# Optimization experiments

Measured on AMD Instinct MI355X. Metric: run time of the kernel, lower is better.

The kernel has to match this reference:

```python
import math
import jax, jax.numpy as jnp
import numpy as np

B, C, H, W = 16, 128, 128, 128  # width == dim required by nn.LayerNorm(dim) on (b,c,h,w)
HEADS, DIM_HEAD = 8, 32
INNER = HEADS * DIM_HEAD


def _ln_last(x, g, b, eps=1e-5):
    # torch nn.LayerNorm over the LAST axis (here: width), biased variance
    mu = x.mean(-1, keepdims=True)
    var = x.var(-1, keepdims=True)
    return (x - mu) * jax.lax.rsqrt(var + eps) * g + b


def setup_inputs() -> dict:
    key = jax.random.key(0)
    k0, k1, k2 = jax.random.split(key, 3)
    return {
        "fmap": jax.random.normal(k0, (B, C, H, W), jnp.float32),
        "ln0_g": jnp.ones((C,), jnp.float32),
        "ln0_b": jnp.zeros((C,), jnp.float32),
        "w_qkv": jax.random.normal(k1, (3 * INNER, C), jnp.float32) * 0.05,
        "w_out": jax.random.normal(k2, (C, INNER), jnp.float32) * 0.05,
        "ln1_g": jnp.ones((C,), jnp.float32),
        "ln1_b": jnp.zeros((C,), jnp.float32),
    }


def reference(fmap, ln0_g, ln0_b, w_qkv, w_out, ln1_g, ln1_b):
    b, c, x, y = fmap.shape
    n = x * y
    scale = DIM_HEAD ** -0.5

    fm = _ln_last(fmap, ln0_g, ln0_b)
    # 1x1 conv (no bias) == channel matmul
    qkv = jnp.einsum('bcxy,oc->boxy', fm, w_qkv)  # (b, 3*inner, x, y)
    q, k, v = jnp.split(qkv, 3, axis=1)

    def to_heads(t):
        # b (h c) x y -> (b h) (x y) c
        return t.reshape(b, HEADS, DIM_HEAD, n).transpose(0, 1, 3, 2).reshape(b * HEADS, n, DIM_HEAD)

    q, k, v = map(to_heads, (q, k, v))

    q = jax.nn.softmax(q, axis=-1) * scale
    k = jax.nn.softmax(k, axis=-2)
    # l2norm(v) along feature dim (F.normalize, eps=1e-12)
    v = v / jnp.clip(jnp.linalg.norm(v, axis=-1, keepdims=True), 1e-12)
    inv = 1.0 / math.sqrt(n)
    k = k * inv
    v = v * inv

    context = jnp.einsum('bnd,bne->bde', k, v)   # small (d=32, e=32) context
    out = jnp.einsum('bnd,bde->bne', q, context)

    # (b h) (x y) d -> b (h d) x y
    out = out.reshape(b, HEADS, n, DIM_HEAD).transpose(0, 1, 3, 2).reshape(b, INNER, x, y)
    out = jax.nn.gelu(out, approximate=False)  # torch nn.GELU default (erf)
    out = jnp.einsum('bcxy,oc->boxy', out, w_out)  # 1x1 conv, no bias
    return _ln_last(out, ln1_g, ln1_b)
```

## Files before the change

kernel.cpp:

```cpp
#include <hip/hip_runtime.h>
#include <math.h>

#define OFF_MU    0u
#define OFF_RSTD  262144u
#define OFF_CTXA  524288u
#define OFF_CTXP  2686976u
#define OFF_WSPL  2883584u
#define OFF_WQSPL 2981888u
#define OFF_WOSPL 3031040u

typedef __attribute__((ext_vector_type(8))) short bf16x8;
typedef __attribute__((ext_vector_type(4))) float f32x4;

__device__ __forceinline__ void split3(float v, unsigned& h, unsigned& m, unsigned& l) {
  unsigned u = __float_as_uint(v);
  float r1 = v - __uint_as_float(u & 0xffff0000u);
  unsigned u1 = __float_as_uint(r1);
  float r2 = r1 - __uint_as_float(u1 & 0xffff0000u);
  h = u >> 16; m = u1 >> 16; l = __float_as_uint(r2) >> 16;
}

__device__ __forceinline__ f32x4 mfma6(const bf16x8& A0, const bf16x8& A1, const bf16x8& A2,
                                       const bf16x8& B0, const bf16x8& B1, const bf16x8& B2,
                                       f32x4 c) {
  c = __builtin_amdgcn_mfma_f32_16x16x32_bf16(A0, B0, c, 0, 0, 0);
  c = __builtin_amdgcn_mfma_f32_16x16x32_bf16(A0, B1, c, 0, 0, 0);
  c = __builtin_amdgcn_mfma_f32_16x16x32_bf16(A1, B0, c, 0, 0, 0);
  c = __builtin_amdgcn_mfma_f32_16x16x32_bf16(A0, B2, c, 0, 0, 0);
  c = __builtin_amdgcn_mfma_f32_16x16x32_bf16(A1, B1, c, 0, 0, 0);
  c = __builtin_amdgcn_mfma_f32_16x16x32_bf16(A2, B0, c, 0, 0, 0);
  return c;
}

__global__ void prep_kernel(const float* __restrict__ wqkv,
                            const float* __restrict__ wout,
                            float* __restrict__ ws) {
  int idx = blockIdx.x * 256 + threadIdx.x;
  float v;
  unsigned short* wp;
  unsigned plane, slot;
  if (idx < 65536) {
    int row = idx >> 7, c = idx & 127;
    int blk = row >> 7, ol = row & 127;
    int hh = (ol >> 5) & 1;
    int src = ((ol & 64) ? 512 : 256) + (2 * blk + hh) * 32 + (ol & 31);
    v = wqkv[src * 128 + c];
    wp = (unsigned short*)(ws + OFF_WSPL);
    plane = 65536; slot = (unsigned)idx;
  } else if (idx < 98304) {
    int j = idx - 65536;
    v = wqkv[j];
    wp = (unsigned short*)(ws + OFF_WQSPL);
    plane = 32768; slot = (unsigned)j;
  } else {
    int j = idx - 98304;
    int o = j >> 8, k = j & 255;
    int cp = (k & 0xE0) | (((k >> 2) & 1) << 4) | (((k >> 3) & 3) << 2) | (k & 3);
    v = wout[o * 256 + cp];
    wp = (unsigned short*)(ws + OFF_WOSPL);
    plane = 32768; slot = (unsigned)j;
  }
  unsigned h, m, l;
  split3(v, h, m, l);
  wp[slot]             = (unsigned short)h;
  wp[plane + slot]     = (unsigned short)m;
  wp[2 * plane + slot] = (unsigned short)l;
}

__launch_bounds__(512, 4)
__global__ void kv_ctx_kernel(const float* __restrict__ fmap,
                              const float* __restrict__ g0,
                              const float* __restrict__ b0,
                              float* __restrict__ ws) {
  __shared__ float sm[13888];
  const int x = blockIdx.x, b = blockIdx.y, t = threadIdx.x;
  const int wave = t >> 6, lane = t & 63;
  const int ln = lane & 15, kb = lane >> 4;
  const int or2 = wave >> 1, yc = wave & 1;
  const int dt = lane >> 3, et = lane & 7;
  const int xg = x >> 3;

  float* pb  = sm;
  float* vb  = sm + 2304;
  float* vss = sm + 4608;
  float* ser = sm + 4864;
  float* rnS = sm + 5120;
  float* red = sm + 5184;
  float* pls = sm + 5184;
  float* muS = sm + 13376;
  float* rsS = sm + 13504;
  float* g0S = sm + 13632;
  float* b0S = sm + 13760;
  float* fmS = sm;

  {
    const int r = t >> 2, q = t & 3;
    const float* p = fmap + (((size_t)(b * 128 + r)) * 128 + x) * 128 + q * 32;
    double s = 0.0, qq = 0.0;
    #pragma unroll
    for (int i = 0; i < 8; ++i) {
      float4 v4 = *(const float4*)(p + i * 4);
      s  += (double)v4.x + (double)v4.y + (double)v4.z + (double)v4.w;
      qq += (double)v4.x * v4.x + (double)v4.y * v4.y
          + (double)v4.z * v4.z + (double)v4.w * v4.w;
    }
    s += __shfl_xor(s, 1); qq += __shfl_xor(qq, 1);
    s += __shfl_xor(s, 2); qq += __shfl_xor(qq, 2);
    if (q == 0) {
      double mu = s * (1.0 / 128.0);
      double var = qq * (1.0 / 128.0) - mu * mu;
      float muf = (float)mu, rsf = (float)(1.0 / sqrt(var + 1e-5));
      muS[r] = muf; rsS[r] = rsf;
      ws[OFF_MU + (unsigned)((b * 128 + r) * 128 + x)] = muf;
      ws[OFF_RSTD + (unsigned)((b * 128 + r) * 128 + x)] = rsf;
    }
  }
  if (t < 128) { g0S[t] = g0[t]; b0S[t] = b0[t]; }

  const unsigned short* wspl = (const unsigned short*)(ws + OFF_WSPL);

  for (int blk = 0; blk < 4; ++blk) {
    f32x4 acc[2][4];
    #pragma unroll
    for (int i = 0; i < 2; ++i)
      #pragma unroll
      for (int j = 0; j < 4; ++j) acc[i][j] = (f32x4){0.f, 0.f, 0.f, 0.f};

    for (int cc = 0; cc < 4; ++cc) {
      bf16x8 af[2][3];
      #pragma unroll
      for (int ot = 0; ot < 2; ++ot)
        #pragma unroll
        for (int p = 0; p < 3; ++p)
          af[ot][p] = *(const bf16x8*)(wspl + p * 65536 +
              ((blk * 128 + or2 * 32 + ot * 16 + ln) * 128 + cc * 32 + kb * 8));

      __syncthreads();
      #pragma unroll
      for (int it = 0; it < 2; ++it) {
        int idx4 = it * 512 + t;
        int c = idx4 >> 5, y4 = (idx4 & 31) * 4;
        int cg = cc * 32 + c;
        const float4 r = *(const float4*)(fmap + (((size_t)(b * 128 + cg)) * 128 + x) * 128 + y4);
        float mu = muS[cg], rs = rsS[cg];
        float4 g = *(const float4*)(g0S + y4);
        float4 be = *(const float4*)(b0S + y4);
        float4 o;
        o.x = (r.x - mu) * rs * g.x + be.x;
        o.y = (r.y - mu) * rs * g.y + be.y;
        o.z = (r.z - mu) * rs * g.z + be.z;
        o.w = (r.w - mu) * rs * g.w + be.w;
        *(float4*)(fmS + c * 128 + y4) = o;
      }
      __syncthreads();
      {
        const int ty = t & 127, cg = t >> 7;
        unsigned int d0[4], d1[4], d2[4];
        #pragma unroll
        for (int jj = 0; jj < 4; ++jj) {
          unsigned int h[2], m[2], l[2];
          #pragma unroll
          for (int e = 0; e < 2; ++e) {
            float v = fmS[(cg * 8 + jj * 2 + e) * 128 + ty];
            split3(v, h[e], m[e], l[e]);
          }
          d0[jj] = h[0] | (h[1] << 16);
          d1[jj] = m[0] | (m[1] << 16);
          d2[jj] = l[0] | (l[1] << 16);
        }
        float* pp = pls + ty * 20 + cg * 4;
        *reinterpret_cast<uint4*>(pp)        = make_uint4(d0[0], d0[1], d0[2], d0[3]);
        *reinterpret_cast<uint4*>(pp + 2560) = make_uint4(d1[0], d1[1], d1[2], d1[3]);
        *reinterpret_cast<uint4*>(pp + 5120) = make_uint4(d2[0], d2[1], d2[2], d2[3]);
      }
      __syncthreads();
      #pragma unroll
      for (int yt = 0; yt < 4; ++yt) {
        const float* bp = pls + ((yc * 4 + yt) * 16 + ln) * 20 + kb * 4;
        bf16x8 B0 = *(const bf16x8*)(bp);
        bf16x8 B1 = *(const bf16x8*)(bp + 2560);
        bf16x8 B2 = *(const bf16x8*)(bp + 5120);
        #pragma unroll
        for (int ot = 0; ot < 2; ++ot)
          acc[ot][yt] = mfma6(af[ot][0], af[ot][1], af[ot][2], B0, B1, B2, acc[ot][yt]);
      }
    }

    for (int hh = 0; hh < 2; ++hh) {
      float u[16], se[4];
      #pragma unroll
      for (int i = 0; i < 16; ++i) u[i] = 0.0f;
      se[0] = se[1] = se[2] = se[3] = 0.0f;

      for (int hf = 0; hf < 2; ++hf) {
        if (wave == hh * 2 + hf) {
          #pragma unroll
          for (int ot = 0; ot < 2; ++ot)
            #pragma unroll
            for (int yt = 0; yt < 4; ++yt) {
              f32x4 a = acc[ot][yt];
              float4 p;
              p.x = __expf(a[0]); p.y = __expf(a[1]);
              p.z = __expf(a[2]); p.w = __expf(a[3]);
              *(float4*)(pb + (yt * 16 + ln) * 36 + ot * 16 + kb * 4) = p;
            }
        }
        if (wave == 4 + hh * 2 + hf) {
          #pragma unroll
          for (int yt = 0; yt < 4; ++yt) {
            f32x4 a0 = acc[0][yt], a1 = acc[1][yt];
            int yl = yt * 16 + ln;
            *(float4*)(vb + yl * 36 + kb * 4)      = make_float4(a0[0], a0[1], a0[2], a0[3]);
            *(float4*)(vb + yl * 36 + 16 + kb * 4) = make_float4(a1[0], a1[1], a1[2], a1[3]);
            float s = a0[0] * a0[0] + a0[1] * a0[1] + a0[2] * a0[2] + a0[3] * a0[3]
                    + a1[0] * a1[0] + a1[1] * a1[1] + a1[2] * a1[2] + a1[3] * a1[3];
            vss[kb * 64 + yl] = s;
          }
        }
        __syncthreads();
        if (t < 64) {
          float s2 = vss[t] + vss[64 + t] + vss[128 + t] + vss[192 + t];
          rnS[t] = 1.0f / fmaxf(sqrtf(s2), 1e-12f);
        }
        __syncthreads();
        #pragma unroll 2
        for (int yy = 0; yy < 8; ++yy) {
          int y = wave * 8 + yy;
          const float4 p = *(const float4*)(pb + y * 36 + dt * 4);
          float4 v = *(const float4*)(vb + y * 36 + et * 4);
          float rn = rnS[y];
          v.x *= rn; v.y *= rn; v.z *= rn; v.w *= rn;
          se[0] += p.x; se[1] += p.y; se[2] += p.z; se[3] += p.w;
          u[0]  = fmaf(p.x, v.x, u[0]);  u[1]  = fmaf(p.x, v.y, u[1]);
          u[2]  = fmaf(p.x, v.z, u[2]);  u[3]  = fmaf(p.x, v.w, u[3]);
          u[4]  = fmaf(p.y, v.x, u[4]);  u[5]  = fmaf(p.y, v.y, u[5]);
          u[6]  = fmaf(p.y, v.z, u[6]);  u[7]  = fmaf(p.y, v.w, u[7]);
          u[8]  = fmaf(p.z, v.x, u[8]);  u[9]  = fmaf(p.z, v.y, u[9]);
          u[10] = fmaf(p.z, v.z, u[10]); u[11] = fmaf(p.z, v.w, u[11]);
          u[12] = fmaf(p.w, v.x, u[12]); u[13] = fmaf(p.w, v.y, u[13]);
          u[14] = fmaf(p.w, v.z, u[14]); u[15] = fmaf(p.w, v.w, u[15]);
        }
        __syncthreads();
      }
      *(float4*)(red + t * 16 + 0)  = make_float4(u[0], u[1], u[2], u[3]);
      *(float4*)(red + t * 16 + 4)  = make_float4(u[4], u[5], u[6], u[7]);
      *(float4*)(red + t * 16 + 8)  = make_float4(u[8], u[9], u[10], u[11]);
      *(float4*)(red + t * 16 + 12) = make_float4(u[12], u[13], u[14], u[15]);
      if (et == 0)
        *(float4*)(ser + (wave * 8 + dt) * 4) = make_float4(se[0], se[1], se[2], se[3]);
      __syncthreads();
      {
        const int tile = t >> 3;
        const int i0 = (t & 7) * 2;
        float s0 = 0.0f, s1 = 0.0f;
        #pragma unroll
        for (int w = 0; w < 8; ++w) {
          s0 += red[(w * 64 + tile) * 16 + i0];
          s1 += red[(w * 64 + tile) * 16 + i0 + 1];
        }
        const int d = (tile >> 3) * 4 + (i0 >> 2);
        const int e = (tile & 7) * 4 + (i0 & 3);
        float* ca = ws + OFF_CTXA + ((size_t)(b * 8 + blk * 2 + hh) * 16 + xg) * 1056;
        atomicAdd(ca + d * 32 + e, s0);
        atomicAdd(ca + d * 32 + e + 1, s1);
        if (t < 32) {
          float ss = 0.0f;
          #pragma unroll
          for (int w = 0; w < 8; ++w) ss += ser[(w * 8 + (t >> 2)) * 4 + (t & 3)];
          atomicAdd(ca + 1024 + t, ss);
        }
      }
    }
  }
}

__global__ void ctx_reduce_kernel(float* __restrict__ ws) {
  __shared__ float sume[32];
  const int bh = blockIdx.x, t = threadIdx.x;
  const float* ca = ws + OFF_CTXA + (size_t)bh * 16 * 1056;
  if (t < 32) {
    double a = 0.0;
    #pragma unroll
    for (int xg = 0; xg < 16; ++xg) a += ca[xg * 1056 + 1024 + t];
    sume[t] = (float)a;
  }
  __syncthreads();
  const double sb = (1.0 / 16384.0) * 0.17677669529663688;
  unsigned short* cp = (unsigned short*)(ws + OFF_CTXP) + (size_t)bh * 3072;
  #pragma unroll
  for (int i = 0; i < 4; ++i) {
    int de = t + 256 * i;
    int d = de >> 5, e = de & 31;
    double a = 0.0;
    #pragma unroll
    for (int xg = 0; xg < 16; ++xg) a += ca[xg * 1056 + de];
    float v = (float)(a * sb / (double)sume[d]);
    int k = ((d >> 2) & 3) * 8 + ((d >> 4) & 1) * 4 + (d & 3);
    unsigned h, m, l;
    split3(v, h, m, l);
    cp[e * 32 + k]        = (unsigned short)h;
    cp[1024 + e * 32 + k] = (unsigned short)m;
    cp[2048 + e * 32 + k] = (unsigned short)l;
  }
}

__launch_bounds__(512, 2)
__global__ void final_kernel(const float* __restrict__ fmap,
                             const float* __restrict__ g0,
                             const float* __restrict__ b0,
                             const float* __restrict__ g1,
                             const float* __restrict__ b1,
                             const float* __restrict__ ws,
                             float* __restrict__ out) {
  __shared__ float sm[14592];
  const int x = blockIdx.x, b = blockIdx.y, t = threadIdx.x;
  const int wave = t >> 6, lane = t & 63;
  const int ln = lane & 15, kb = lane >> 4;
  const int or2 = wave >> 1, yc = wave & 1;

  float* fmS = sm;
  float* pls = sm + 4096;
  float* gel = sm;
  float* muS = sm + 13824;
  float* rsS = sm + 13952;
  float* g0S = sm + 14080;
  float* b0S = sm + 14208;
  float* lnm = sm + 14336;
  float* lnr = sm + 14464;

  if (t < 128) {
    muS[t] = ws[OFF_MU + (unsigned)((b * 128 + t) * 128 + x)];
    rsS[t] = ws[OFF_RSTD + (unsigned)((b * 128 + t) * 128 + x)];
  } else if (t < 256) g0S[t - 128] = g0[t - 128];
  else if (t < 384) b0S[t - 256] = b0[t - 256];

  const unsigned short* wqspl = (const unsigned short*)(ws + OFF_WQSPL);
  const unsigned short* wospl = (const unsigned short*)(ws + OFF_WOSPL);
  const unsigned short* ctxp  = (const unsigned short*)(ws + OFF_CTXP);

  f32x4 oacc[2][4];
  #pragma unroll
  for (int i = 0; i < 2; ++i)
    #pragma unroll
    for (int j = 0; j < 4; ++j) oacc[i][j] = (f32x4){0.f, 0.f, 0.f, 0.f};

  for (int qblk = 0; qblk < 2; ++qblk) {
    f32x4 qacc[2][4];
    #pragma unroll
    for (int i = 0; i < 2; ++i)
      #pragma unroll
      for (int j = 0; j < 4; ++j) qacc[i][j] = (f32x4){0.f, 0.f, 0.f, 0.f};

    for (int cc = 0; cc < 4; ++cc) {
      bf16x8 af[2][3];
      #pragma unroll
      for (int ot = 0; ot < 2; ++ot)
        #pragma unroll
        for (int p = 0; p < 3; ++p)
          af[ot][p] = *(const bf16x8*)(wqspl + p * 32768 +
              ((qblk * 128 + or2 * 32 + ot * 16 + ln) * 128 + cc * 32 + kb * 8));

      __syncthreads();
      #pragma unroll
      for (int it = 0; it < 2; ++it) {
        int idx4 = it * 512 + t;
        int c = idx4 >> 5, y4 = (idx4 & 31) * 4;
        int cg = cc * 32 + c;
        const float4 r = *(const float4*)(fmap + (((size_t)(b * 128 + cg)) * 128 + x) * 128 + y4);
        float mu = muS[cg], rs = rsS[cg];
        float4 g = *(const float4*)(g0S + y4);
        float4 be = *(const float4*)(b0S + y4);
        float4 o;
        o.x = (r.x - mu) * rs * g.x + be.x;
        o.y = (r.y - mu) * rs * g.y + be.y;
        o.z = (r.z - mu) * rs * g.z + be.z;
        o.w = (r.w - mu) * rs * g.w + be.w;
        *(float4*)(fmS + c * 128 + y4) = o;
      }
      __syncthreads();
      {
        const int ty = t & 127, cg = t >> 7;
        unsigned int d0[4], d1[4], d2[4];
        #pragma unroll
        for (int jj = 0; jj < 4; ++jj) {
          unsigned int h[2], m[2], l[2];
          #pragma unroll
          for (int e = 0; e < 2; ++e) {
            float v = fmS[(cg * 8 + jj * 2 + e) * 128 + ty];
            split3(v, h[e], m[e], l[e]);
          }
          d0[jj] = h[0] | (h[1] << 16);
          d1[jj] = m[0] | (m[1] << 16);
          d2[jj] = l[0] | (l[1] << 16);
        }
        float* pp = pls + ty * 20 + cg * 4;
        *reinterpret_cast<uint4*>(pp)        = make_uint4(d0[0], d0[1], d0[2], d0[3]);
        *reinterpret_cast<uint4*>(pp + 2560) = make_uint4(d1[0], d1[1], d1[2], d1[3]);
        *reinterpret_cast<uint4*>(pp + 5120) = make_uint4(d2[0], d2[1], d2[2], d2[3]);
      }
      __syncthreads();
      #pragma unroll
      for (int yt = 0; yt < 4; ++yt) {
        const float* bp = pls + ((yc * 4 + yt) * 16 + ln) * 20 + kb * 4;
        bf16x8 B0 = *(const bf16x8*)(bp);
        bf16x8 B1 = *(const bf16x8*)(bp + 2560);
        bf16x8 B2 = *(const bf16x8*)(bp + 5120);
        #pragma unroll
        for (int ot = 0; ot < 2; ++ot)
          qacc[ot][yt] = mfma6(af[ot][0], af[ot][1], af[ot][2], B0, B1, B2, qacc[ot][yt]);
      }
    }

    float rssum[4];
    bf16x8 pf0[4], pf1[4], pf2[4];
    #pragma unroll
    for (int yt = 0; yt < 4; ++yt) {
      float pv[8];
      #pragma unroll
      for (int ot = 0; ot < 2; ++ot)
        #pragma unroll
        for (int r = 0; r < 4; ++r)
          pv[ot * 4 + r] = __expf(qacc[ot][yt][r]);
      float ps = ((pv[0] + pv[1]) + (pv[2] + pv[3])) + ((pv[4] + pv[5]) + (pv[6] + pv[7]));
      ps += __shfl_xor(ps, 16);
      ps += __shfl_xor(ps, 32);
      rssum[yt] = 1.0f / ps;
      unsigned wh[4], wm[4], wl[4];
      #pragma unroll
      for (int j = 0; j < 4; ++j) {
        unsigned h0, m0, l0, h1, m1, l1;
        split3(pv[2 * j], h0, m0, l0);
        split3(pv[2 * j + 1], h1, m1, l1);
        wh[j] = h0 | (h1 << 16);
        wm[j] = m0 | (m1 << 16);
        wl[j] = l0 | (l1 << 16);
      }
      uint4 uh = make_uint4(wh[0], wh[1], wh[2], wh[3]);
      uint4 um = make_uint4(wm[0], wm[1], wm[2], wm[3]);
      uint4 ul = make_uint4(wl[0], wl[1], wl[2], wl[3]);
      pf0[yt] = *(const bf16x8*)&uh;
      pf1[yt] = *(const bf16x8*)&um;
      pf2[yt] = *(const bf16x8*)&ul;
    }

    f32x4 ge[2][4];
    const unsigned short* chp = ctxp + (size_t)(b * 8 + qblk * 4 + or2) * 3072;
    #pragma unroll
    for (int ot = 0; ot < 2; ++ot) {
      bf16x8 aq0 = *(const bf16x8*)(chp +        (ot * 16 + ln) * 32 + kb * 8);
      bf16x8 aq1 = *(const bf16x8*)(chp + 1024 + (ot * 16 + ln) * 32 + kb * 8);
      bf16x8 aq2 = *(const bf16x8*)(chp + 2048 + (ot * 16 + ln) * 32 + kb * 8);
      #pragma unroll
      for (int yt = 0; yt < 4; ++yt) {
        f32x4 c = (f32x4){0.f, 0.f, 0.f, 0.f};
        ge[ot][yt] = mfma6(aq0, aq1, aq2, pf0[yt], pf1[yt], pf2[yt], c);
      }
    }

    #pragma unroll
    for (int ot = 0; ot < 2; ++ot)
      #pragma unroll
      for (int yt = 0; yt < 4; ++yt)
        #pragma unroll
        for (int r = 0; r < 4; ++r) {
          float v = ge[ot][yt][r] * rssum[yt];
          ge[ot][yt][r] = 0.5f * v * (1.0f + erff(v * 0.70710678118654752f));
        }

    for (int ph = 0; ph < 2; ++ph) {
      __syncthreads();
      if ((or2 >> 1) == ph) {
        const int c16 = (or2 & 1) * 16;
        #pragma unroll
        for (int yt = 0; yt < 4; ++yt) {
          float* grow = gel + ((yc * 4 + yt) * 16 + ln) * 36 + c16 + kb * 4;
          #pragma unroll
          for (int ot = 0; ot < 2; ++ot) {
            unsigned h0, m0, l0, h1, m1, l1, h2, m2, l2, h3, m3, l3;
            split3(ge[ot][yt][0], h0, m0, l0);
            split3(ge[ot][yt][1], h1, m1, l1);
            split3(ge[ot][yt][2], h2, m2, l2);
            split3(ge[ot][yt][3], h3, m3, l3);
            *(uint2*)(grow + ot * 2)        = make_uint2(h0 | (h1 << 16), h2 | (h3 << 16));
            *(uint2*)(grow + 4608 + ot * 2) = make_uint2(m0 | (m1 << 16), m2 | (m3 << 16));
            *(uint2*)(grow + 9216 + ot * 2) = make_uint2(l0 | (l1 << 16), l2 | (l3 << 16));
          }
        }
      }
      __syncthreads();
      #pragma unroll
      for (int kc = 0; kc < 2; ++kc) {
        bf16x8 ao[2][3];
        #pragma unroll
        for (int ot = 0; ot < 2; ++ot)
          #pragma unroll
          for (int p = 0; p < 3; ++p)
            ao[ot][p] = *(const bf16x8*)(wospl + p * 32768 +
                ((or2 * 32 + ot * 16 + ln) * 256 + qblk * 128 + ph * 64 + kc * 32 + kb * 8));
        #pragma unroll
        for (int yt = 0; yt < 4; ++yt) {
          const float* bp = gel + ((yc * 4 + yt) * 16 + ln) * 36 + kc * 16 + kb * 4;
          bf16x8 B0 = *(const bf16x8*)(bp);
          bf16x8 B1 = *(const bf16x8*)(bp + 4608);
          bf16x8 B2 = *(const bf16x8*)(bp + 9216);
          #pragma unroll
          for (int ot = 0; ot < 2; ++ot)
            oacc[ot][yt] = mfma6(ao[ot][0], ao[ot][1], ao[ot][2], B0, B1, B2, oacc[ot][yt]);
        }
      }
    }
  }

  __syncthreads();
  float* red_s = sm;
  float* red_q = sm + 4096;
  #pragma unroll
  for (int ot = 0; ot < 2; ++ot)
    #pragma unroll
    for (int r = 0; r < 4; ++r) {
      int o = or2 * 32 + ot * 16 + kb * 4 + r;
      float s = 0.0f, q = 0.0f;
      #pragma unroll
      for (int yt = 0; yt < 4; ++yt) { float v = oacc[ot][yt][r]; s += v; q = fmaf(v, v, q); }
      red_s[o * 32 + yc * 16 + ln] = s;
      red_q[o * 32 + yc * 16 + ln] = q;
    }
  __syncthreads();
  if (t < 128) {
    double s = 0.0, q = 0.0;
    #pragma unroll
    for (int i = 0; i < 32; ++i) { s += red_s[t * 32 + i]; q += red_q[t * 32 + i]; }
    double mu = s * (1.0 / 128.0);
    double var = q * (1.0 / 128.0) - mu * mu;
    lnm[t] = (float)mu;
    lnr[t] = (float)(1.0 / sqrt(var + 1e-5));
  }
  __syncthreads();
  float g1v[4], b1v[4];
  #pragma unroll
  for (int yt = 0; yt < 4; ++yt) {
    int y = (yc * 4 + yt) * 16 + ln;
    g1v[yt] = g1[y]; b1v[yt] = b1[y];
  }
  #pragma unroll
  for (int ot = 0; ot < 2; ++ot)
    #pragma unroll
    for (int r = 0; r < 4; ++r) {
      int o = or2 * 32 + ot * 16 + kb * 4 + r;
      float mu = lnm[o], rs = lnr[o];
      #pragma unroll
      for (int yt = 0; yt < 4; ++yt) {
        int y = (yc * 4 + yt) * 16 + ln;
        out[(((size_t)(b * 128 + o)) * 128 + x) * 128 + y] =
            (oacc[ot][yt][r] - mu) * rs * g1v[yt] + b1v[yt];
      }
    }
}

extern "C" void kernel_launch(void* const* d_in, const int* in_sizes, int n_in,
                              void* d_out, int out_size, void* d_ws, size_t ws_size,
                              hipStream_t stream) {
  const float* fmap = (const float*)d_in[0];
  const float* g0   = (const float*)d_in[1];
  const float* b0   = (const float*)d_in[2];
  const float* wqkv = (const float*)d_in[3];
  const float* wout = (const float*)d_in[4];
  const float* g1   = (const float*)d_in[5];
  const float* b1   = (const float*)d_in[6];
  float* ws  = (float*)d_ws;
  float* out = (float*)d_out;

  hipMemsetAsync((char*)d_ws + (size_t)OFF_CTXA * 4, 0, (size_t)2162688 * 4, stream);
  prep_kernel<<<512, 256, 0, stream>>>(wqkv, wout, ws);
  kv_ctx_kernel<<<dim3(128, 16), 512, 0, stream>>>(fmap, g0, b0, ws);
  ctx_reduce_kernel<<<128, 256, 0, stream>>>(ws);
  final_kernel<<<dim3(128, 16), 512, 0, stream>>>(fmap, g0, b0, g1, b1, ws, out);
}
```

Measured before the change: 883.9 us.

## Compute all KV blocks in one pass over fmap and process two heads per step

The kv_ctx kernel now keeps accumulators for all four k/v output blocks in registers, so each fmap chunk is loaded, layer-normalised and split into bf16 planes once instead of four times. The softmax/context stage then handles two heads at once, using all 8 waves over 32 rows each, which halves the number of barrier-separated phases. To fit this, launch bounds drop to 2 blocks per SM and shared memory grows to about 80KB. The cost is higher register pressure (32 accumulator vectors) and lower occupancy.

Measured after the change: 872.3 us. About the same (-1.3%).

```diff
diff --git a/kernel.cpp b/kernel.cpp
--- a/kernel.cpp
+++ b/kernel.cpp
@@ -67,12 +67,12 @@
   wp[2 * plane + slot] = (unsigned short)l;
 }
 
-__launch_bounds__(512, 4)
+__launch_bounds__(512, 2)
 __global__ void kv_ctx_kernel(const float* __restrict__ fmap,
                               const float* __restrict__ g0,
                               const float* __restrict__ b0,
                               float* __restrict__ ws) {
-  __shared__ float sm[13888];
+  __shared__ float sm[19968];
   const int x = blockIdx.x, b = blockIdx.y, t = threadIdx.x;
   const int wave = t >> 6, lane = t & 63;
   const int ln = lane & 15, kb = lane >> 4;
@@ -80,18 +80,18 @@
   const int dt = lane >> 3, et = lane & 7;
   const int xg = x >> 3;
 
+  float* fmS = sm;
+  float* pls = sm + 4096;
+  float* muS = sm + 11776;
+  float* rsS = sm + 11904;
+  float* g0S = sm + 12032;
+  float* b0S = sm + 12160;
   float* pb  = sm;
-  float* vb  = sm + 2304;
-  float* vss = sm + 4608;
-  float* ser = sm + 4864;
-  float* rnS = sm + 5120;
-  float* red = sm + 5184;
-  float* pls = sm + 5184;
-  float* muS = sm + 13376;
-  float* rsS = sm + 13504;
-  float* g0S = sm + 13632;
-  float* b0S = sm + 13760;
-  float* fmS = sm;
+  float* vb  = sm + 9216;
+  float* vss = sm + 18432;
+  float* rnS = sm + 19456;
+  float* ser = sm + 19712;
+  float* red = sm;
 
   {
     const int r = t >> 2, q = t & 3;
@@ -119,12 +119,263 @@
 
   const unsigned short* wspl = (const unsigned short*)(ws + OFF_WSPL);
 
+  f32x4 acc[4][2][4];
+  #pragma unroll
+  for (int k = 0; k < 4; ++k)
+    #pragma unroll
+    for (int i = 0; i < 2; ++i)
+      #pragma unroll
+      for (int j = 0; j < 4; ++j) acc[k][i][j] = (f32x4){0.f, 0.f, 0.f, 0.f};
+
+  for (int cc = 0; cc < 4; ++cc) {
+    __syncthreads();
+    #pragma unroll
+    for (int it = 0; it < 2; ++it) {
+      int idx4 = it * 512 + t;
+      int c = idx4 >> 5, y4 = (idx4 & 31) * 4;
+      int cg = cc * 32 + c;
+      const float4 r = *(const float4*)(fmap + (((size_t)(b * 128 + cg)) * 128 + x) * 128 + y4);
+      float mu = muS[cg], rs = rsS[cg];
+      float4 g = *(const float4*)(g0S + y4);
+      float4 be = *(const float4*)(b0S + y4);
+      float4 o;
+      o.x = (r.x - mu) * rs * g.x + be.x;
+      o.y = (r.y - mu) * rs * g.y + be.y;
+      o.z = (r.z - mu) * rs * g.z + be.z;
+      o.w = (r.w - mu) * rs * g.w + be.w;
+      *(float4*)(fmS + c * 128 + y4) = o;
+    }
+    __syncthreads();
+    {
+      const int ty = t & 127, cg = t >> 7;
+      unsigned int d0[4], d1[4], d2[4];
+      #pragma unroll
+      for (int jj = 0; jj < 4; ++jj) {
+        unsigned int h[2], m[2], l[2];
+        #pragma unroll
+        for (int e = 0; e < 2; ++e) {
+          float v = fmS[(cg * 8 + jj * 2 + e) * 128 + ty];
+          split3(v, h[e], m[e], l[e]);
+        }
+        d0[jj] = h[0] | (h[1] << 16);
+        d1[jj] = m[0] | (m[1] << 16);
+        d2[jj] = l[0] | (l[1] << 16);
+      }
+      float* pp = pls + ty * 20 + cg * 4;
+      *reinterpret_cast<uint4*>(pp)        = make_uint4(d0[0], d0[1], d0[2], d0[3]);
+      *reinterpret_cast<uint4*>(pp + 2560) = make_uint4(d1[0], d1[1], d1[2], d1[3]);
+      *reinterpret_cast<uint4*>(pp + 5120) = make_uint4(d2[0], d2[1], d2[2], d2[3]);
+    }
+    __syncthreads();
+    #pragma unroll
+    for (int pg = 0; pg < 2; ++pg) {
+      bf16x8 af[2][2][3];
+      #pragma unroll
+      for (int bb = 0; bb < 2; ++bb)
+        #pragma unroll
+        for (int ot = 0; ot < 2; ++ot)
+          #pragma unroll
+          for (int p = 0; p < 3; ++p)
+            af[bb][ot][p] = *(const bf16x8*)(wspl + p * 65536 +
+                (((pg * 2 + bb) * 128 + or2 * 32 + ot * 16 + ln) * 128 + cc * 32 + kb * 8));
+      #pragma unroll
+      for (int yt = 0; yt < 4; ++yt) {
+        const float* bp = pls + ((yc * 4 + yt) * 16 + ln) * 20 + kb * 4;
+        bf16x8 B0 = *(const bf16x8*)(bp);
+        bf16x8 B1 = *(const bf16x8*)(bp + 2560);
+        bf16x8 B2 = *(const bf16x8*)(bp + 5120);
+        #pragma unroll
+        for (int bb = 0; bb < 2; ++bb)
+          #pragma unroll
+          for (int ot = 0; ot < 2; ++ot)
+            acc[pg * 2 + bb][ot][yt] =
+                mfma6(af[bb][ot][0], af[bb][ot][1], af[bb][ot][2], B0, B1, B2,
+                      acc[pg * 2 + bb][ot][yt]);
+      }
+    }
+  }
+
+  #pragma unroll
   for (int blk = 0; blk < 4; ++blk) {
-    f32x4 acc[2][4];
+    __syncthreads();
+    if (or2 < 2) {
+      const int h = or2;
+      #pragma unroll
+      for (int ot = 0; ot < 2; ++ot)
+        #pragma unroll
+        for (int yt = 0; yt < 4; ++yt) {
+          f32x4 a = acc[blk][ot][yt];
+          float4 p;
+          p.x = __expf(a[0]); p.y = __expf(a[1]);
+          p.z = __expf(a[2]); p.w = __expf(a[3]);
+          *(float4*)(pb + h * 4608 + ((yc * 4 + yt) * 16 + ln) * 36 + ot * 16 + kb * 4) = p;
+        }
+    } else {
+      const int h = or2 - 2;
+      #pragma unroll
+      for (int yt = 0; yt < 4; ++yt) {
+        f32x4 a0 = acc[blk][0][yt], a1 = acc[blk][1][yt];
+        int y = (yc * 4 + yt) * 16 + ln;
+        *(float4*)(vb + h * 4608 + y * 36 + kb * 4)      = make_float4(a0[0], a0[1], a0[2], a0[3]);
+        *(float4*)(vb + h * 4608 + y * 36 + 16 + kb * 4) = make_float4(a1[0], a1[1], a1[2], a1[3]);
+        float s = a0[0] * a0[0] + a0[1] * a0[1] + a0[2] * a0[2] + a0[3] * a0[3]
+                + a1[0] * a1[0] + a1[1] * a1[1] + a1[2] * a1[2] + a1[3] * a1[3];
+        vss[h * 512 + kb * 128 + y] = s;
+      }
+    }
+    __syncthreads();
+    if (t < 256) {
+      int h = t >> 7, y = t & 127;
+      const float* vh = vss + h * 512;
+      float s2 = vh[y] + vh[128 + y] + vh[256 + y] + vh[384 + y];
+      rnS[h * 128 + y] = 1.0f / fmaxf(sqrtf(s2), 1e-12f);
+    }
+    __syncthreads();
+    float u[16], se[4];
+    #pragma unroll
+    for (int i = 0; i < 16; ++i) u[i] = 0.0f;
+    se[0] = se[1] = se[2] = se[3] = 0.0f;
+    {
+      const int h = wave >> 2, yb = (wave & 3) * 32;
+      const float* pbh = pb + h * 4608;
+      const float* vbh = vb + h * 4608;
+      const float* rnh = rnS + h * 128;
+      #pragma unroll 4
+      for (int yy = 0; yy < 32; ++yy) {
+        int y = yb + yy;
+        const float4 p = *(const float4*)(pbh + y * 36 + dt * 4);
+        float4 v = *(const float4*)(vbh + y * 36 + et * 4);
+        float rn = rnh[y];
+        v.x *= rn; v.y *= rn; v.z *= rn; v.w *= rn;
+        se[0] += p.x; se[1] += p.y; se[2] += p.z; se[3] += p.w;
+        u[0]  = fmaf(p.x, v.x, u[0]);  u[1]  = fmaf(p.x, v.y, u[1]);
+        u[2]  = fmaf(p.x, v.z, u[2]);  u[3]  = fmaf(p.x, v.w, u[3]);
+        u[4]  = fmaf(p.y, v.x, u[4]);  u[5]  = fmaf(p.y, v.y, u[5]);
+        u[6]  = fmaf(p.y, v.z, u[6]);  u[7]  = fmaf(p.y, v.w, u[7]);
+        u[8]  = fmaf(p.z, v.x, u[8]);  u[9]  = fmaf(p.z, v.y, u[9]);
+        u[10] = fmaf(p.z, v.z, u[10]); u[11] = fmaf(p.z, v.w, u[11]);
+        u[12] = fmaf(p.w, v.x, u[12]); u[13] = fmaf(p.w, v.y, u[13]);
+        u[14] = fmaf(p.w, v.z, u[14]); u[15] = fmaf(p.w, v.w, u[15]);
+      }
+    }
+    __syncthreads();
+    {
+      const int h = wave >> 2;
+      float* rp = red + h * 4096 + ((wave & 3) * 64 + lane) * 16;
+      *(float4*)(rp + 0)  = make_float4(u[0], u[1], u[2], u[3]);
+      *(float4*)(rp + 4)  = make_float4(u[4], u[5], u[6], u[7]);
+      *(float4*)(rp + 8)  = make_float4(u[8], u[9], u[10], u[11]);
+      *(float4*)(rp + 12) = make_float4(u[12], u[13], u[14], u[15]);
+      if (et == 0)
+        *(float4*)(ser + h * 128 + ((wave & 3) * 8 + dt) * 4) = make_float4(se[0], se[1], se[2], se[3]);
+    }
+    __syncthreads();
+    {
+      const int tile = t >> 3, i0 = (t & 7) * 2;
+      const int d = (tile >> 3) * 4 + (i0 >> 2);
+      const int e = (tile & 7) * 4 + (i0 & 3);
+      #pragma unroll
+      for (int h = 0; h < 2; ++h) {
+        const float* rh = red + h * 4096;
+        float s0 = 0.0f, s1 = 0.0f;
+        #pragma unroll
+        for (int w4 = 0; w4 < 4; ++w4) {
+          s0 += rh[(w4 * 64 + tile) * 16 + i0];
+          s1 += rh[(w4 * 64 + tile) * 16 + i0 + 1];
+        }
+        float* ca = ws + OFF_CTXA + ((size_t)(b * 8 + blk * 2 + h) * 16 + xg) * 1056;
+        atomicAdd(ca + d * 32 + e, s0);
+        atomicAdd(ca + d * 32 + e + 1, s1);
+      }
+      if (t < 64) {
+        int h = t >> 5, tq = t & 31;
+        float ss = 0.0f;
+        #pragma unroll
+        for (int w4 = 0; w4 < 4; ++w4)
+          ss += ser[h * 128 + (w4 * 8 + (tq >> 2)) * 4 + (tq & 3)];
+        float* ca = ws + OFF_CTXA + ((size_t)(b * 8 + blk * 2 + h) * 16 + xg) * 1056;
+        atomicAdd(ca + 1024 + tq, ss);
+      }
+    }
+  }
+}
+
+__global__ void ctx_reduce_kernel(float* __restrict__ ws) {
+  __shared__ float sume[32];
+  const int bh = blockIdx.x, t = threadIdx.x;
+  const float* ca = ws + OFF_CTXA + (size_t)bh * 16 * 1056;
+  if (t < 32) {
+    double a = 0.0;
+    #pragma unroll
+    for (int xg = 0; xg < 16; ++xg) a += ca[xg * 1056 + 1024 + t];
+    sume[t] = (float)a;
+  }
+  __syncthreads();
+  const double sb = (1.0 / 16384.0) * 0.17677669529663688;
+  unsigned short* cp = (unsigned short*)(ws + OFF_CTXP) + (size_t)bh * 3072;
+  #pragma unroll
+  for (int i = 0; i < 4; ++i) {
+    int de = t + 256 * i;
+    int d = de >> 5, e = de & 31;
+    double a = 0.0;
+    #pragma unroll
+    for (int xg = 0; xg < 16; ++xg) a += ca[xg * 1056 + de];
+    float v = (float)(a * sb / (double)sume[d]);
+    int k = ((d >> 2) & 3) * 8 + ((d >> 4) & 1) * 4 + (d & 3);
+    unsigned h, m, l;
+    split3(v, h, m, l);
+    cp[e * 32 + k]        = (unsigned short)h;
+    cp[1024 + e * 32 + k] = (unsigned short)m;
+    cp[2048 + e * 32 + k] = (unsigned short)l;
+  }
+}
+
+__launch_bounds__(512, 2)
+__global__ void final_kernel(const float* __restrict__ fmap,
+                             const float* __restrict__ g0,
+                             const float* __restrict__ b0,
+                             const float* __restrict__ g1,
+                             const float* __restrict__ b1,
+                             const float* __restrict__ ws,
+                             float* __restrict__ out) {
+  __shared__ float sm[14592];
+  const int x = blockIdx.x, b = blockIdx.y, t = threadIdx.x;
+  const int wave = t >> 6, lane = t & 63;
+  const int ln = lane & 15, kb = lane >> 4;
+  const int or2 = wave >> 1, yc = wave & 1;
+
+  float* fmS = sm;
+  float* pls = sm + 4096;
+  float* gel = sm;
+  float* muS = sm + 13824;
+  float* rsS = sm + 13952;
+  float* g0S = sm + 14080;
+  float* b0S = sm + 14208;
+  float* lnm = sm + 14336;
+  float* lnr = sm + 14464;
+
+  if (t < 128) {
+    muS[t] = ws[OFF_MU + (unsigned)((b * 128 + t) * 128 + x)];
+    rsS[t] = ws[OFF_RSTD + (unsigned)((b * 128 + t) * 128 + x)];
+  } else if (t < 256) g0S[t - 128] = g0[t - 128];
+  else if (t < 384) b0S[t - 256] = b0[t - 256];
+
+  const unsigned short* wqspl = (const unsigned short*)(ws + OFF_WQSPL);
+  const unsigned short* wospl = (const unsigned short*)(ws + OFF_WOSPL);
+  const unsigned short* ctxp  = (const unsigned short*)(ws + OFF_CTXP);
+
+  f32x4 oacc[2][4];
+  #pragma unroll
+  for (int i = 0; i < 2; ++i)
+    #pragma unroll
+    for (int j = 0; j < 4; ++j) oacc[i][j] = (f32x4){0.f, 0.f, 0.f, 0.f};
+
+  for (int qblk = 0; qblk < 2; ++qblk) {
+    f32x4 qacc[2][4];
     #pragma unroll
     for (int i = 0; i < 2; ++i)
       #pragma unroll
-      for (int j = 0; j < 4; ++j) acc[i][j] = (f32x4){0.f, 0.f, 0.f, 0.f};
+      for (int j = 0; j < 4; ++j) qacc[i][j] = (f32x4){0.f, 0.f, 0.f, 0.f};
 
     for (int cc = 0; cc < 4; ++cc) {
       bf16x8 af[2][3];
@@ -132,8 +383,8 @@
       for (int ot = 0; ot < 2; ++ot)
         #pragma unroll
         for (int p = 0; p < 3; ++p)
-          af[ot][p] = *(const bf16x8*)(wspl + p * 65536 +
-              ((blk * 128 + or2 * 32 + ot * 16 + ln) * 128 + cc * 32 + kb * 8));
+          af[ot][p] = *(const bf16x8*)(wqspl + p * 32768 +
+              ((qblk * 128 + or2 * 32 + ot * 16 + ln) * 128 + cc * 32 + kb * 8));
 
       __syncthreads();
       #pragma unroll
@@ -182,231 +433,6 @@
         bf16x8 B2 = *(const bf16x8*)(bp + 5120);
         #pragma unroll
         for (int ot = 0; ot < 2; ++ot)
-          acc[ot][yt] = mfma6(af[ot][0], af[ot][1], af[ot][2], B0, B1, B2, acc[ot][yt]);
-      }
-    }
-
-    for (int hh = 0; hh < 2; ++hh) {
-      float u[16], se[4];
-      #pragma unroll
-      for (int i = 0; i < 16; ++i) u[i] = 0.0f;
-      se[0] = se[1] = se[2] = se[3] = 0.0f;
-
-      for (int hf = 0; hf < 2; ++hf) {
-        if (wave == hh * 2 + hf) {
-          #pragma unroll
-          for (int ot = 0; ot < 2; ++ot)
-            #pragma unroll
-            for (int yt = 0; yt < 4; ++yt) {
-              f32x4 a = acc[ot][yt];
-              float4 p;
-              p.x = __expf(a[0]); p.y = __expf(a[1]);
-              p.z = __expf(a[2]); p.w = __expf(a[3]);
-              *(float4*)(pb + (yt * 16 + ln) * 36 + ot * 16 + kb * 4) = p;
-            }
-        }
-        if (wave == 4 + hh * 2 + hf) {
-          #pragma unroll
-          for (int yt = 0; yt < 4; ++yt) {
-            f32x4 a0 = acc[0][yt], a1 = acc[1][yt];
-            int yl = yt * 16 + ln;
-            *(float4*)(vb + yl * 36 + kb * 4)      = make_float4(a0[0], a0[1], a0[2], a0[3]);
-            *(float4*)(vb + yl * 36 + 16 + kb * 4) = make_float4(a1[0], a1[1], a1[2], a1[3]);
-            float s = a0[0] * a0[0] + a0[1] * a0[1] + a0[2] * a0[2] + a0[3] * a0[3]
-                    + a1[0] * a1[0] + a1[1] * a1[1] + a1[2] * a1[2] + a1[3] * a1[3];
-            vss[kb * 64 + yl] = s;
-          }
-        }
-        __syncthreads();
-        if (t < 64) {
-          float s2 = vss[t] + vss[64 + t] + vss[128 + t] + vss[192 + t];
-          rnS[t] = 1.0f / fmaxf(sqrtf(s2), 1e-12f);
-        }
-        __syncthreads();
-        #pragma unroll 2
-        for (int yy = 0; yy < 8; ++yy) {
-          int y = wave * 8 + yy;
-          const float4 p = *(const float4*)(pb + y * 36 + dt * 4);
-          float4 v = *(const float4*)(vb + y * 36 + et * 4);
-          float rn = rnS[y];
-          v.x *= rn; v.y *= rn; v.z *= rn; v.w *= rn;
-          se[0] += p.x; se[1] += p.y; se[2] += p.z; se[3] += p.w;
-          u[0]  = fmaf(p.x, v.x, u[0]);  u[1]  = fmaf(p.x, v.y, u[1]);
-          u[2]  = fmaf(p.x, v.z, u[2]);  u[3]  = fmaf(p.x, v.w, u[3]);
-          u[4]  = fmaf(p.y, v.x, u[4]);  u[5]  = fmaf(p.y, v.y, u[5]);
-          u[6]  = fmaf(p.y, v.z, u[6]);  u[7]  = fmaf(p.y, v.w, u[7]);
-          u[8]  = fmaf(p.z, v.x, u[8]);  u[9]  = fmaf(p.z, v.y, u[9]);
-          u[10] = fmaf(p.z, v.z, u[10]); u[11] = fmaf(p.z, v.w, u[11]);
-          u[12] = fmaf(p.w, v.x, u[12]); u[13] = fmaf(p.w, v.y, u[13]);
-          u[14] = fmaf(p.w, v.z, u[14]); u[15] = fmaf(p.w, v.w, u[15]);
-        }
-        __syncthreads();
-      }
-      *(float4*)(red + t * 16 + 0)  = make_float4(u[0], u[1], u[2], u[3]);
-      *(float4*)(red + t * 16 + 4)  = make_float4(u[4], u[5], u[6], u[7]);
-      *(float4*)(red + t * 16 + 8)  = make_float4(u[8], u[9], u[10], u[11]);
-      *(float4*)(red + t * 16 + 12) = make_float4(u[12], u[13], u[14], u[15]);
-      if (et == 0)
-        *(float4*)(ser + (wave * 8 + dt) * 4) = make_float4(se[0], se[1], se[2], se[3]);
-      __syncthreads();
-      {
-        const int tile = t >> 3;
-        const int i0 = (t & 7) * 2;
-        float s0 = 0.0f, s1 = 0.0f;
-        #pragma unroll
-        for (int w = 0; w < 8; ++w) {
-          s0 += red[(w * 64 + tile) * 16 + i0];
-          s1 += red[(w * 64 + tile) * 16 + i0 + 1];
-        }
-        const int d = (tile >> 3) * 4 + (i0 >> 2);
-        const int e = (tile & 7) * 4 + (i0 & 3);
-        float* ca = ws + OFF_CTXA + ((size_t)(b * 8 + blk * 2 + hh) * 16 + xg) * 1056;
-        atomicAdd(ca + d * 32 + e, s0);
-        atomicAdd(ca + d * 32 + e + 1, s1);
-        if (t < 32) {
-          float ss = 0.0f;
-          #pragma unroll
-          for (int w = 0; w < 8; ++w) ss += ser[(w * 8 + (t >> 2)) * 4 + (t & 3)];
-          atomicAdd(ca + 1024 + t, ss);
-        }
-      }
-    }
-  }
-}
-
-__global__ void ctx_reduce_kernel(float* __restrict__ ws) {
-  __shared__ float sume[32];
-  const int bh = blockIdx.x, t = threadIdx.x;
-  const float* ca = ws + OFF_CTXA + (size_t)bh * 16 * 1056;
-  if (t < 32) {
-    double a = 0.0;
-    #pragma unroll
-    for (int xg = 0; xg < 16; ++xg) a += ca[xg * 1056 + 1024 + t];
-    sume[t] = (float)a;
-  }
-  __syncthreads();
-  const double sb = (1.0 / 16384.0) * 0.17677669529663688;
-  unsigned short* cp = (unsigned short*)(ws + OFF_CTXP) + (size_t)bh * 3072;
-  #pragma unroll
-  for (int i = 0; i < 4; ++i) {
-    int de = t + 256 * i;
-    int d = de >> 5, e = de & 31;
-    double a = 0.0;
-    #pragma unroll
-    for (int xg = 0; xg < 16; ++xg) a += ca[xg * 1056 + de];
-    float v = (float)(a * sb / (double)sume[d]);
-    int k = ((d >> 2) & 3) * 8 + ((d >> 4) & 1) * 4 + (d & 3);
-    unsigned h, m, l;
-    split3(v, h, m, l);
-    cp[e * 32 + k]        = (unsigned short)h;
-    cp[1024 + e * 32 + k] = (unsigned short)m;
-    cp[2048 + e * 32 + k] = (unsigned short)l;
-  }
-}
-
-__launch_bounds__(512, 2)
-__global__ void final_kernel(const float* __restrict__ fmap,
-                             const float* __restrict__ g0,
-                             const float* __restrict__ b0,
-                             const float* __restrict__ g1,
-                             const float* __restrict__ b1,
-                             const float* __restrict__ ws,
-                             float* __restrict__ out) {
-  __shared__ float sm[14592];
-  const int x = blockIdx.x, b = blockIdx.y, t = threadIdx.x;
-  const int wave = t >> 6, lane = t & 63;
-  const int ln = lane & 15, kb = lane >> 4;
-  const int or2 = wave >> 1, yc = wave & 1;
-
-  float* fmS = sm;
-  float* pls = sm + 4096;
-  float* gel = sm;
-  float* muS = sm + 13824;
-  float* rsS = sm + 13952;
-  float* g0S = sm + 14080;
-  float* b0S = sm + 14208;
-  float* lnm = sm + 14336;
-  float* lnr = sm + 14464;
-
-  if (t < 128) {
-    muS[t] = ws[OFF_MU + (unsigned)((b * 128 + t) * 128 + x)];
-    rsS[t] = ws[OFF_RSTD + (unsigned)((b * 128 + t) * 128 + x)];
-  } else if (t < 256) g0S[t - 128] = g0[t - 128];
-  else if (t < 384) b0S[t - 256] = b0[t - 256];
-
-  const unsigned short* wqspl = (const unsigned short*)(ws + OFF_WQSPL);
-  const unsigned short* wospl = (const unsigned short*)(ws + OFF_WOSPL);
-  const unsigned short* ctxp  = (const unsigned short*)(ws + OFF_CTXP);
-
-  f32x4 oacc[2][4];
-  #pragma unroll
-  for (int i = 0; i < 2; ++i)
-    #pragma unroll
-    for (int j = 0; j < 4; ++j) oacc[i][j] = (f32x4){0.f, 0.f, 0.f, 0.f};
-
-  for (int qblk = 0; qblk < 2; ++qblk) {
-    f32x4 qacc[2][4];
-    #pragma unroll
-    for (int i = 0; i < 2; ++i)
-      #pragma unroll
-      for (int j = 0; j < 4; ++j) qacc[i][j] = (f32x4){0.f, 0.f, 0.f, 0.f};
-
-    for (int cc = 0; cc < 4; ++cc) {
-      bf16x8 af[2][3];
-      #pragma unroll
-      for (int ot = 0; ot < 2; ++ot)
-        #pragma unroll
-        for (int p = 0; p < 3; ++p)
-          af[ot][p] = *(const bf16x8*)(wqspl + p * 32768 +
-              ((qblk * 128 + or2 * 32 + ot * 16 + ln) * 128 + cc * 32 + kb * 8));
-
-      __syncthreads();
-      #pragma unroll
-      for (int it = 0; it < 2; ++it) {
-        int idx4 = it * 512 + t;
-        int c = idx4 >> 5, y4 = (idx4 & 31) * 4;
-        int cg = cc * 32 + c;
-        const float4 r = *(const float4*)(fmap + (((size_t)(b * 128 + cg)) * 128 + x) * 128 + y4);
-        float mu = muS[cg], rs = rsS[cg];
-        float4 g = *(const float4*)(g0S + y4);
-        float4 be = *(const float4*)(b0S + y4);
-        float4 o;
-        o.x = (r.x - mu) * rs * g.x + be.x;
-        o.y = (r.y - mu) * rs * g.y + be.y;
-        o.z = (r.z - mu) * rs * g.z + be.z;
-        o.w = (r.w - mu) * rs * g.w + be.w;
-        *(float4*)(fmS + c * 128 + y4) = o;
-      }
-      __syncthreads();
-      {
-        const int ty = t & 127, cg = t >> 7;
-        unsigned int d0[4], d1[4], d2[4];
-        #pragma unroll
-        for (int jj = 0; jj < 4; ++jj) {
-          unsigned int h[2], m[2], l[2];
-          #pragma unroll
-          for (int e = 0; e < 2; ++e) {
-            float v = fmS[(cg * 8 + jj * 2 + e) * 128 + ty];
-            split3(v, h[e], m[e], l[e]);
-          }
-          d0[jj] = h[0] | (h[1] << 16);
-          d1[jj] = m[0] | (m[1] << 16);
-          d2[jj] = l[0] | (l[1] << 16);
-        }
-        float* pp = pls + ty * 20 + cg * 4;
-        *reinterpret_cast<uint4*>(pp)        = make_uint4(d0[0], d0[1], d0[2], d0[3]);
-        *reinterpret_cast<uint4*>(pp + 2560) = make_uint4(d1[0], d1[1], d1[2], d1[3]);
-        *reinterpret_cast<uint4*>(pp + 5120) = make_uint4(d2[0], d2[1], d2[2], d2[3]);
-      }
-      __syncthreads();
-      #pragma unroll
-      for (int yt = 0; yt < 4; ++yt) {
-        const float* bp = pls + ((yc * 4 + yt) * 16 + ln) * 20 + kb * 4;
-        bf16x8 B0 = *(const bf16x8*)(bp);
-        bf16x8 B1 = *(const bf16x8*)(bp + 2560);
-        bf16x8 B2 = *(const bf16x8*)(bp + 5120);
-        #pragma unroll
-        for (int ot = 0; ot < 2; ++ot)
           qacc[ot][yt] = mfma6(af[ot][0], af[ot][1], af[ot][2], B0, B1, B2, qacc[ot][yt]);
       }
     }
```
